# Performance work log

Hardware: AMD Instinct MI355X
Metric: run time of the kernel (lower is better)

## Reference

```python
import jax, jax.numpy as jnp
import numpy as np

B, S, H, NH, DW, V, W, L, NL = 8, 512, 768, 12, 300, 100000, 256, 4, 2


def _make_word_index(seed=0):
    # contiguous, non-overlapping spans of length 1..L starting at pos 1,
    # zero-padded at the end (matches the `break` on (0,0) in the original).
    rng = np.random.default_rng(seed)
    wi = np.zeros((B, W, 2), np.int32)
    for b in range(B):
        pos, w = 1, 0
        while w < W and pos < S:
            n = int(rng.integers(1, L + 1))
            end = min(pos + n, S)
            wi[b, w] = (pos, end)
            pos, w = end, w + 1
    return jnp.asarray(wi)


def _lin(key, din, dout):
    kw, _ = jax.random.split(key)
    return jax.random.normal(kw, (din, dout), jnp.float32) * 0.02, jnp.zeros((dout,), jnp.float32)


def setup_inputs() -> dict:
    key = jax.random.key(0)
    ks = jax.random.split(key, 14)
    tbl = jax.random.normal(ks[2], (V + 1, DW), jnp.float32) * 0.1
    tbl = tbl.at[V].set(0.0)  # appended zero row for OOV/pad
    d = dict(
        sequence_output=jax.random.normal(ks[0], (B, S, H), jnp.float32),
        word_ids=jax.random.randint(ks[1], (B, W), 0, V),
        word_index=_make_word_index(),
        word_table=tbl,
        mix_lambda=jnp.asarray(0.5, jnp.float32),
        mu=jnp.asarray(0.5, jnp.float32),
    )
    d['dt_w'], d['dt_b'] = _lin(ks[3], DW, H)
    d['dr_w'], d['dr_b'] = _lin(ks[4], H, H)
    d['q_w'], d['q_b'] = _lin(ks[5], H, H)
    d['k_w'], d['k_b'] = _lin(ks[6], H, H)
    d['v_w'], d['v_b'] = _lin(ks[7], H, H)
    d['qi_w'], d['qi_b'] = _lin(ks[8], H, H)
    d['ki_w'], d['ki_b'] = _lin(ks[9], H, H)
    d['vi_w'], d['vi_b'] = _lin(ks[10], H, H)
    d['fus_w'], d['fus_b'] = _lin(ks[11], H, H)
    d['dense_w'], d['dense_b'] = _lin(ks[12], H, H)
    d['cls_w'], d['cls_b'] = _lin(ks[13], H, NL)
    return d


def _mhsa(x, wq, bq, wk, bk, wv, bv, bias=None):
    b, s, h = x.shape
    hd = h // NH
    q = (x @ wq + bq).reshape(b, s, NH, hd).transpose(0, 2, 1, 3)
    k = (x @ wk + bk).reshape(b, s, NH, hd).transpose(0, 2, 1, 3)
    v = (x @ wv + bv).reshape(b, s, NH, hd).transpose(0, 2, 1, 3)
    scores = jnp.einsum('bhqd,bhkd->bhqk', q, k) / jnp.sqrt(jnp.asarray(hd, x.dtype))
    if bias is not None:
        scores = scores + bias
    p = jax.nn.softmax(scores, axis=-1)
    return jnp.einsum('bhqk,bhkd->bhqd', p, v).transpose(0, 2, 1, 3).reshape(b, s, h)


def _forward(sequence_output, word_ids, word_index, word_table, dt_w, dt_b, dr_w, dr_b,
             mix_lambda, mu, q_w, q_b, k_w, k_b, v_w, v_b, qi_w, qi_b, ki_w, ki_b,
             vi_w, vi_b, fus_w, fus_b, dense_w, dense_b, cls_w, cls_b):
    x = sequence_output
    # word embedding -> dim_transform -> tanh -> dim_retain
    we = jnp.tanh(word_table[word_ids] @ dt_w + dt_b) @ dr_w + dr_b  # [B,W,H]
    starts, ends = word_index[..., 0], word_index[..., 1]
    n = ends - starts                     # word lengths, 0 for padding
    valid_w = n > 0
    lpos = jnp.arange(L)
    pos = jnp.clip(starts[..., None] + lpos, 0, S - 1)              # [B,W,L]
    cvalid = (lpos[None, None, :] < n[..., None]) & valid_w[..., None]
    bidx = jnp.arange(B)[:, None, None]
    # char-word cosine similarity (computed on the ORIGINAL sequence_output)
    xg = x[bidx, pos]                                               # [B,W,L,H]
    xn = xg / jnp.linalg.norm(xg, axis=-1, keepdims=True)
    wen = we / jnp.linalg.norm(we, axis=-1, keepdims=True)
    cos = jnp.sum(xn * wen[:, :, None, :], axis=-1)                 # [B,W,L]
    cos_m = jnp.where(cvalid, cos, -1e9)
    # add softmax(cos)-weighted word embedding onto chars (scatter-add)
    sm = jax.nn.softmax(cos_m, axis=-1) * cvalid
    x1 = x.at[bidx, pos].add(sm[..., None] * we[:, :, None, :])
    # ragged mix: most-important char (mic) per word
    mic = jnp.argmax(cos_m, axis=-1)                                # [B,W]
    x1g = x1[bidx, pos]                                             # [B,W,L,H]
    x_mic = x1g[jnp.arange(B)[:, None], jnp.arange(W)[None, :], mic]  # [B,W,H]
    sum_x = jnp.sum(x1g * cvalid[..., None], axis=2)                # [B,W,H]
    f = jnp.exp(mix_lambda - 1.0)
    a = (1.0 - f) / jnp.maximum(n - 1, 1).astype(x.dtype)           # [B,W]
    mix_other = (1.0 - a[..., None, None]) * x1g + a[..., None, None] * x_mic[:, :, None, :]
    mix_mic = f * x_mic + a[..., None] * (sum_x - x_mic)
    is_mic = lpos[None, None, :] == mic[:, :, None]
    newv = jnp.where(is_mic[..., None], mix_mic[:, :, None, :], mix_other)
    mixmask = (cvalid & (n > 1)[..., None])[..., None].astype(x.dtype)
    x_mix = x1.at[bidx, pos].add((newv - x1g) * mixmask)
    # importance attention mask: only mic (or the single char) columns visible
    keep_pos = jnp.where(n == 1, starts, jnp.clip(starts + mic, 0, S - 1))
    keep = jnp.zeros((B, S), bool).at[jnp.arange(B)[:, None], keep_pos].max(valid_w)
    bias = jnp.where(keep[:, None, None, :], 0.0, -jnp.inf).astype(x.dtype)  # [B,1,1,S]
    h1 = _mhsa(x_mix, q_w, q_b, k_w, k_b, v_w, v_b, None)
    h2 = _mhsa(x_mix, qi_w, qi_b, ki_w, ki_b, vi_w, vi_b, bias)
    fus = jnp.tanh((mu * h1 + (1.0 - mu) * h2) @ fus_w + fus_b)
    pooled = jnp.tanh(fus[:, 0] @ dense_w + dense_b)                # CLS pooling
    return pooled @ cls_w + cls_b                                   # [B,NL]


def reference(sequence_output, word_ids, word_index, word_table, dt_w, dt_b, dr_w, dr_b,
              mix_lambda, mu, q_w, q_b, k_w, k_b, v_w, v_b, qi_w, qi_b, ki_w, ki_b,
              vi_w, vi_b, fus_w, fus_b, dense_w, dense_b, cls_w, cls_b):
    return _forward(sequence_output, word_ids, word_index, word_table, dt_w, dt_b, dr_w, dr_b,
                    mix_lambda, mu, q_w, q_b, k_w, k_b, v_w, v_b, qi_w, qi_b, ki_w, ki_b,
                    vi_w, vi_b, fus_w, fus_b, dense_w, dense_b, cls_w, cls_b)
```

## Files before the change

### kernel.cpp

```cpp
#include <hip/hip_runtime.h>
#include <math.h>

#define NB 8
#define SS 512
#define HH 768
#define NHD 12
#define HDIM 64
#define DWD 300
#define WW 256
#define LL 4
#define KC 6

__device__ __forceinline__ float waveReduceSum(float v){
    #pragma unroll
    for(int o=32;o>0;o>>=1) v += __shfl_xor(v,o,64);
    return v;
}

__global__ __launch_bounds__(256) void k_embed1f(const float* __restrict__ table,
        const int* __restrict__ ids, const float* __restrict__ Wm,
        const float* __restrict__ bias, float* __restrict__ out,
        int* __restrict__ keep,
        const float* __restrict__ x, const float* __restrict__ qw,
        const float* __restrict__ qiw, float* __restrict__ qpart){
    int bid = blockIdx.x;
    int t = threadIdx.x;
    if(bid >= 400){
        int rb = bid - 400;
        int kc = rb % KC;
        int jt = (rb/KC) % 3;
        int b  = rb / (KC*3);
        int j = jt*256 + t;
        const float* x0 = x + (size_t)b*SS*HH;
        int i0 = kc*128;
        float a1=0.f, a2=0.f;
        for(int i=i0;i<i0+128;i++){
            float xv = x0[i];
            a1 += xv*qw[(size_t)i*HH+j];
            a2 += xv*qiw[(size_t)i*HH+j];
        }
        qpart[(((size_t)kc*NB + b)*2 + 0)*HH + j] = a1;
        qpart[(((size_t)kc*NB + b)*2 + 1)*HH + j] = a2;
        return;
    }
    if(bid >= 384){
        int i = (bid-384)*256 + t;
        if(i < NB*SS) keep[i] = 0;
        return;
    }
    const int K=300, NT=19;
    __shared__ float As[16][68];
    __shared__ float Bs[16][68];
    int bx = bid % 12;
    int by = bid / 12;
    int m0 = by*64, n0 = bx*64;
    int tm = t>>4, tn = t&15;
    int lm = t>>2, lk = (t&3)*4;
    int kk = t>>4, c4 = (t&15)*4;
    int row_id = ids[m0+lm];
    const float* arow = table + (size_t)row_id*DWD;
    float acc[4][4] = {};
    float4 av, bv;
    if(lk < K) av = *(const float4*)&arow[lk]; else av = make_float4(0,0,0,0);
    if(kk < K) bv = *(const float4*)&Wm[(size_t)kk*HH + n0 + c4]; else bv = make_float4(0,0,0,0);
    for(int kt=0;kt<NT;kt++){
        __syncthreads();
        As[lk+0][lm]=av.x; As[lk+1][lm]=av.y; As[lk+2][lm]=av.z; As[lk+3][lm]=av.w;
        *(float4*)&Bs[kk][c4] = bv;
        __syncthreads();
        if(kt+1 < NT){
            int k0 = (kt+1)*16;
            if(k0+lk < K) av = *(const float4*)&arow[k0+lk]; else av = make_float4(0,0,0,0);
            if(k0+kk < K) bv = *(const float4*)&Wm[(size_t)(k0+kk)*HH + n0 + c4]; else bv = make_float4(0,0,0,0);
        }
        #pragma unroll
        for(int k=0;k<16;k++){
            float4 a = *(const float4*)&As[k][tm*4];
            float4 b = *(const float4*)&Bs[k][tn*4];
            acc[0][0]+=a.x*b.x; acc[0][1]+=a.x*b.y; acc[0][2]+=a.x*b.z; acc[0][3]+=a.x*b.w;
            acc[1][0]+=a.y*b.x; acc[1][1]+=a.y*b.y; acc[1][2]+=a.y*b.z; acc[1][3]+=a.y*b.w;
            acc[2][0]+=a.z*b.x; acc[2][1]+=a.z*b.y; acc[2][2]+=a.z*b.z; acc[2][3]+=a.z*b.w;
            acc[3][0]+=a.w*b.x; acc[3][1]+=a.w*b.y; acc[3][2]+=a.w*b.z; acc[3][3]+=a.w*b.w;
        }
    }
    #pragma unroll
    for(int i=0;i<4;i++){
        int m = m0 + tm*4 + i;
        int n = n0 + tn*4;
        float4 o;
        o.x = tanhf(acc[i][0] + bias[n+0]);
        o.y = tanhf(acc[i][1] + bias[n+1]);
        o.z = tanhf(acc[i][2] + bias[n+2]);
        o.w = tanhf(acc[i][3] + bias[n+3]);
        *(float4*)&out[(size_t)m*HH + n] = o;
    }
}

__global__ __launch_bounds__(256) void k_embed2f(const float* __restrict__ A,
        const float* __restrict__ Wm, const float* __restrict__ bias,
        float* __restrict__ out,
        const float4* __restrict__ xin4, float4* __restrict__ xmix4,
        const float* __restrict__ qpart,
        const float* __restrict__ qb, const float* __restrict__ qib,
        const float* __restrict__ kb, const float* __restrict__ kib,
        float* __restrict__ q0g, float* __restrict__ cst){
    int bid = blockIdx.x;
    int t = threadIdx.x;
    if(bid >= 3456){
        int b = bid - 3456;
        __shared__ float q0s[HH], qi0s[HH];
        for(int j=t;j<HH;j+=256){
            float a1=qb[j], a2=qib[j];
            #pragma unroll
            for(int kc=0;kc<KC;kc++){
                a1 += qpart[(((size_t)kc*NB+b)*2+0)*HH+j];
                a2 += qpart[(((size_t)kc*NB+b)*2+1)*HH+j];
            }
            q0s[j]=a1; qi0s[j]=a2;
            q0g[((size_t)b*2+0)*HH+j]=a1;
            q0g[((size_t)b*2+1)*HH+j]=a2;
        }
        __syncthreads();
        if(t<24){
            int slot=t, h=slot%NHD;
            const float* Kb = (slot<NHD)? kb:kib;
            const float* Q  = (slot<NHD)? q0s:qi0s;
            float a=0.f;
            for(int j=0;j<HDIM;j++) a += Kb[h*HDIM+j]*Q[h*HDIM+j];
            cst[b*24+slot]=a;
        }
        return;
    }
    if(bid >= 384){
        int i = (bid-384)*256 + t;
        xmix4[i] = xin4[i];
        return;
    }
    const int NT = 48;
    __shared__ float As[16][68];
    __shared__ float Bs[16][68];
    int bx = bid % 12;
    int by = bid / 12;
    int m0 = by*64, n0 = bx*64;
    int tm = t>>4, tn = t&15;
    int lm = t>>2, lk = (t&3)*4;
    int kk = t>>4, c4 = (t&15)*4;
    const float* arow = A + (size_t)(m0+lm)*HH;
    float acc[4][4] = {};
    float4 av = *(const float4*)&arow[lk];
    float4 bv = *(const float4*)&Wm[(size_t)kk*HH + n0 + c4];
    for(int kt=0;kt<NT;kt++){
        __syncthreads();
        As[lk+0][lm]=av.x; As[lk+1][lm]=av.y; As[lk+2][lm]=av.z; As[lk+3][lm]=av.w;
        *(float4*)&Bs[kk][c4] = bv;
        __syncthreads();
        if(kt+1 < NT){
            int k0 = (kt+1)*16;
            av = *(const float4*)&arow[k0+lk];
            bv = *(const float4*)&Wm[(size_t)(k0+kk)*HH + n0 + c4];
        }
        #pragma unroll
        for(int k=0;k<16;k++){
            float4 a = *(const float4*)&As[k][tm*4];
            float4 b = *(const float4*)&Bs[k][tn*4];
            acc[0][0]+=a.x*b.x; acc[0][1]+=a.x*b.y; acc[0][2]+=a.x*b.z; acc[0][3]+=a.x*b.w;
            acc[1][0]+=a.y*b.x; acc[1][1]+=a.y*b.y; acc[1][2]+=a.y*b.z; acc[1][3]+=a.y*b.w;
            acc[2][0]+=a.z*b.x; acc[2][1]+=a.z*b.y; acc[2][2]+=a.z*b.z; acc[2][3]+=a.z*b.w;
            acc[3][0]+=a.w*b.x; acc[3][1]+=a.w*b.y; acc[3][2]+=a.w*b.z; acc[3][3]+=a.w*b.w;
        }
    }
    #pragma unroll
    for(int i=0;i<4;i++){
        int m = m0 + tm*4 + i;
        int n = n0 + tn*4;
        float4 o;
        o.x = acc[i][0] + bias[n+0];
        o.y = acc[i][1] + bias[n+1];
        o.z = acc[i][2] + bias[n+2];
        o.w = acc[i][3] + bias[n+3];
        *(float4*)&out[(size_t)m*HH + n] = o;
    }
}

__global__ __launch_bounds__(256) void k_cosmix(const float* __restrict__ x,
        const int* __restrict__ wi, const float* __restrict__ we,
        const float* __restrict__ lam, int* __restrict__ keep,
        float* __restrict__ xmix,
        const float* __restrict__ q0g, const float* __restrict__ kw,
        const float* __restrict__ kiw, float* __restrict__ r){
    int bid = blockIdx.x;
    int t = threadIdx.x;
    if(bid >= 2048){
        int rb = bid - 2048;
        int ct = rb % 3;
        int slot = (rb/3) % 24;
        int b = rb / 72;
        int h = slot % NHD;
        __shared__ float qs[HDIM];
        const float* Q = q0g + ((size_t)b*2 + (slot<NHD?0:1))*HH + h*HDIM;
        if(t<HDIM) qs[t] = Q[t];
        __syncthreads();
        const float* K = (slot<NHD)? kw : kiw;
        int c = ct*256 + t;
        const float4* K4 = (const float4*)(K + (size_t)c*HH + h*HDIM);
        const float4* q4 = (const float4*)qs;
        float a=0.f;
        #pragma unroll
        for(int j=0;j<16;j++){
            float4 kv=K4[j], qv=q4[j];
            a += kv.x*qv.x + kv.y*qv.y + kv.z*qv.z + kv.w*qv.w;
        }
        r[((size_t)(b*24+slot))*HH + c] = a;
        return;
    }
    int bw = bid;
    int b = bw >> 8;
    int start = wi[bw*2+0];
    int end   = wi[bw*2+1];
    int n = end - start;
    if(n <= 0) return;
    __shared__ float weS[HH];
    __shared__ float xrow[LL][HH];
    __shared__ float cos_s[LL];
    int wv = t>>6, lane = t&63;
    const float* wer = we + (size_t)bw*HH;
    float wev[12];
    float wn = 0.f;
    #pragma unroll
    for(int i=0;i<12;i++){
        float v = wer[lane+64*i];
        wev[i]=v; wn += v*v;
        if(wv==0) weS[lane+64*i] = v;
    }
    wn = waveReduceSum(wn);
    if(wv < n){
        const float* xr = x + ((size_t)(b*SS + start + wv))*HH;
        float d=0.f, xs=0.f;
        #pragma unroll
        for(int i=0;i<12;i++){
            float xv = xr[lane+64*i];
            xrow[wv][lane+64*i] = xv;
            d += xv*wev[i]; xs += xv*xv;
        }
        d = waveReduceSum(d); xs = waveReduceSum(xs);
        if(lane==0) cos_s[wv] = d / sqrtf(xs*wn);
    } else {
        if(lane==0) cos_s[wv] = -1e9f;
    }
    __syncthreads();
    float c0=cos_s[0], c1=cos_s[1], c2=cos_s[2], c3=cos_s[3];
    float m = fmaxf(fmaxf(c0,c1),fmaxf(c2,c3));
    float e0 = (0<n)? expf(c0-m):0.f;
    float e1 = (1<n)? expf(c1-m):0.f;
    float e2 = (2<n)? expf(c2-m):0.f;
    float e3 = (3<n)? expf(c3-m):0.f;
    float inv = 1.f/(e0+e1+e2+e3);
    float s0=e0*inv, s1=e1*inv, s2=e2*inv, s3=e3*inv;
    int mic = 0; float bv = c0;
    if(c1 > bv){bv=c1;mic=1;}
    if(c2 > bv){bv=c2;mic=2;}
    if(c3 > bv){bv=c3;mic=3;}
    if(t==0) keep[b*SS + start + mic] = 1;
    float f = expf(lam[0] - 1.f);
    float a = (n>1)? (1.f-f)/(float)(n-1) : (1.f-f);
    for(int j=t; j<HH; j+=256){
        float wej = weS[j];
        float v0=0.f,v1=0.f,v2=0.f,v3=0.f;
        if(0<n) v0 = xrow[0][j] + s0*wej;
        if(1<n) v1 = xrow[1][j] + s1*wej;
        if(2<n) v2 = xrow[2][j] + s2*wej;
        if(3<n) v3 = xrow[3][j] + s3*wej;
        float sumx = v0+v1+v2+v3;
        float xm = (mic==0)?v0:(mic==1)?v1:(mic==2)?v2:v3;
        float mm = f*xm + a*(sumx-xm);
        if(0<n) xmix[((size_t)(b*SS+start+0))*HH+j] = (0==mic)? (n==1? v0 : mm) : ((1.f-a)*v0 + a*xm);
        if(1<n) xmix[((size_t)(b*SS+start+1))*HH+j] = (1==mic)? mm : ((1.f-a)*v1 + a*xm);
        if(2<n) xmix[((size_t)(b*SS+start+2))*HH+j] = (2==mic)? mm : ((1.f-a)*v2 + a*xm);
        if(3<n) xmix[((size_t)(b*SS+start+3))*HH+j] = (3==mic)? mm : ((1.f-a)*v3 + a*xm);
    }
}

__global__ __launch_bounds__(256) void k_scores(const float* __restrict__ xmix,
        const float* __restrict__ r, const float* __restrict__ cst,
        const int* __restrict__ keep, float* __restrict__ scores){
    int bs = blockIdx.x;
    int b = bs >> 9, s = bs & 511;
    __shared__ float xr[HH];
    for(int i=threadIdx.x;i<HH;i+=256) xr[i] = xmix[(size_t)bs*HH + i];
    __syncthreads();
    int wv = threadIdx.x>>6, lane = threadIdx.x&63;
    int kp = keep[b*SS + s];
    #pragma unroll
    for(int q=0;q<6;q++){
        int slot = wv*6 + q;
        const float* rr = r + ((size_t)(b*24+slot))*HH;
        float d = 0.f;
        #pragma unroll
        for(int i=0;i<12;i++) d += xr[lane+64*i]*rr[lane+64*i];
        d = waveReduceSum(d);
        if(lane==0){
            float sc = (d + cst[b*24+slot])*0.125f;
            if(slot>=12 && !kp) sc = -1e30f;
            scores[((size_t)(b*24+slot))*SS + s] = sc;
        }
    }
}

__global__ __launch_bounds__(256) void k_attn(const float* __restrict__ scores,
        const float* __restrict__ xmix, float* __restrict__ cg){
    int rb = blockIdx.x;
    int jt = rb % 3;
    int bslot = rb / 3;
    int b = bslot / 24, slot = bslot % 24;
    int t = threadIdx.x;
    __shared__ float p[SS];
    __shared__ float red[256];
    const float* srow = scores + (size_t)bslot*SS;
    float v0 = srow[t], v1 = srow[t+256];
    red[t] = fmaxf(v0,v1); __syncthreads();
    for(int o=128;o>0;o>>=1){ if(t<o) red[t] = fmaxf(red[t],red[t+o]); __syncthreads(); }
    float m = red[0]; __syncthreads();
    float e0 = expf(v0-m), e1 = expf(v1-m);
    red[t] = e0+e1; __syncthreads();
    for(int o=128;o>0;o>>=1){ if(t<o) red[t] += red[t+o]; __syncthreads(); }
    float inv = 1.f/red[0];
    p[t] = e0*inv; p[t+256] = e1*inv;
    __syncthreads();
    int j = jt*256 + t;
    const float* xb = xmix + (size_t)b*SS*HH + j;
    float a0 = 0.f;
    for(int s=0;s<SS;s++) a0 += p[s]*xb[(size_t)s*HH];
    cg[((size_t)bslot)*HH + j] = a0;
    (void)slot;
}

__global__ __launch_bounds__(256) void k_finA(const float* __restrict__ cg,
        const float* __restrict__ vw, const float* __restrict__ viw,
        const float* __restrict__ mu_, float* __restrict__ part){
    int kc = blockIdx.x % KC;
    int jt = (blockIdx.x/KC) % 3;
    int b  = blockIdx.x / (KC*3);
    int j = jt*256 + threadIdx.x;
    int h = j >> 6;
    float mu = mu_[0];
    const float* c1 = cg + ((size_t)(b*24+h))*HH;
    const float* c2 = cg + ((size_t)(b*24+12+h))*HH;
    int i0 = kc*128;
    float a1=0.f, a2=0.f;
    for(int i=i0;i<i0+128;i++){
        a1 += c1[i]*vw[(size_t)i*HH+j];
        a2 += c2[i]*viw[(size_t)i*HH+j];
    }
    part[((size_t)kc*NB+b)*HH + j] = mu*a1 + (1.f-mu)*a2;
}

__global__ __launch_bounds__(256) void k_finB(const float* __restrict__ part1,
        const float* __restrict__ vb, const float* __restrict__ vib,
        const float* __restrict__ mu_, const float* __restrict__ fw,
        float* __restrict__ part2){
    int kc = blockIdx.x % KC;
    int jt = (blockIdx.x/KC) % 3;
    int b  = blockIdx.x / (KC*3);
    int i0 = kc*128;
    int t = threadIdx.x;
    __shared__ float gs[128];
    if(t < 128){
        int i = i0 + t;
        float mu = mu_[0];
        float s = mu*vb[i] + (1.f-mu)*vib[i];
        #pragma unroll
        for(int k2=0;k2<KC;k2++) s += part1[((size_t)k2*NB+b)*HH + i];
        gs[t] = s;
    }
    __syncthreads();
    int j = jt*256 + t;
    float a = 0.f;
    for(int k=0;k<128;k++) a += gs[k]*fw[(size_t)(i0+k)*HH + j];
    part2[((size_t)kc*NB+b)*HH + j] = a;
}

__global__ __launch_bounds__(256) void k_finC(const float* __restrict__ part2,
        const float* __restrict__ fb, const float* __restrict__ dw,
        float* __restrict__ part1){
    int kc = blockIdx.x % KC;
    int jt = (blockIdx.x/KC) % 3;
    int b  = blockIdx.x / (KC*3);
    int i0 = kc*128;
    int t = threadIdx.x;
    __shared__ float fs[128];
    if(t < 128){
        int i = i0 + t;
        float s = fb[i];
        #pragma unroll
        for(int k2=0;k2<KC;k2++) s += part2[((size_t)k2*NB+b)*HH + i];
        fs[t] = tanhf(s);
    }
    __syncthreads();
    int j = jt*256 + t;
    float a = 0.f;
    for(int k=0;k<128;k++) a += fs[k]*dw[(size_t)(i0+k)*HH + j];
    part1[((size_t)kc*NB+b)*HH + j] = a;
}

__global__ __launch_bounds__(256) void k_finD(const float* __restrict__ part,
        const float* __restrict__ db, const float* __restrict__ cw,
        const float* __restrict__ cb, float* __restrict__ out){
    int b = blockIdx.x;
    int t = threadIdx.x;
    __shared__ float pooled[HH];
    __shared__ float red[256];
    for(int j=t;j<HH;j+=256){
        float s = db[j];
        #pragma unroll
        for(int kc=0;kc<KC;kc++) s += part[((size_t)kc*NB+b)*HH+j];
        pooled[j] = tanhf(s);
    }
    __syncthreads();
    float p0=0.f, p1=0.f;
    for(int i=t;i<HH;i+=256){ p0 += pooled[i]*cw[i*2+0]; p1 += pooled[i]*cw[i*2+1]; }
    red[t]=p0; __syncthreads();
    for(int o=128;o>0;o>>=1){ if(t<o) red[t]+=red[t+o]; __syncthreads(); }
    if(t==0) out[b*2+0] = red[0]+cb[0];
    __syncthreads();
    red[t]=p1; __syncthreads();
    for(int o=128;o>0;o>>=1){ if(t<o) red[t]+=red[t+o]; __syncthreads(); }
    if(t==0) out[b*2+1] = red[0]+cb[1];
}

extern "C" void kernel_launch(void* const* d_in, const int* in_sizes, int n_in,
                              void* d_out, int out_size, void* d_ws, size_t ws_size,
                              hipStream_t stream) {
    const float* x          = (const float*)d_in[0];
    const int*   word_ids   = (const int*)  d_in[1];
    const int*   word_index = (const int*)  d_in[2];
    const float* table      = (const float*)d_in[3];
    const float* lam        = (const float*)d_in[4];
    const float* mu         = (const float*)d_in[5];
    const float* dt_w = (const float*)d_in[6];
    const float* dt_b = (const float*)d_in[7];
    const float* dr_w = (const float*)d_in[8];
    const float* dr_b = (const float*)d_in[9];
    const float* q_w  = (const float*)d_in[10];
    const float* q_b  = (const float*)d_in[11];
    const float* k_w  = (const float*)d_in[12];
    const float* k_b  = (const float*)d_in[13];
    const float* v_w  = (const float*)d_in[14];
    const float* v_b  = (const float*)d_in[15];
    const float* qi_w = (const float*)d_in[16];
    const float* qi_b = (const float*)d_in[17];
    const float* ki_w = (const float*)d_in[18];
    const float* ki_b = (const float*)d_in[19];
    const float* vi_w = (const float*)d_in[20];
    const float* vi_b = (const float*)d_in[21];
    const float* fus_w = (const float*)d_in[22];
    const float* fus_b = (const float*)d_in[23];
    const float* dense_w = (const float*)d_in[24];
    const float* dense_b = (const float*)d_in[25];
    const float* cls_w = (const float*)d_in[26];
    const float* cls_b = (const float*)d_in[27];
    float* out = (float*)d_out;

    char* w = (char*)d_ws;
    float* xmix   = (float*)(w + 0);
    float* tbuf   = (float*)(w + 12582912);
    float* we     = (float*)(w + 18874368);
    float* scores = (float*)(w + 25165824);
    float* r      = (float*)(w + 25559040);
    float* cst    = (float*)(w + 26148864);
    int*   keep   = (int*)  (w + 26149888);
    float* cg     = (float*)(w + 26166272);
    float* qpart  = (float*)(w + 26756096);
    float* q0g    = (float*)(w + 27051008);
    float* part1  = (float*)(w + 27100160);
    float* part2  = (float*)(w + 27247616);
    (void)ws_size; (void)in_sizes; (void)n_in; (void)out_size;

    k_embed1f<<<544, 256, 0, stream>>>(table, word_ids, dt_w, dt_b, tbuf, keep,
                                       x, q_w, qi_w, qpart);
    k_embed2f<<<3464, 256, 0, stream>>>(tbuf, dr_w, dr_b, we,
                                        (const float4*)x, (float4*)xmix,
                                        qpart, q_b, qi_b, k_b, ki_b, q0g, cst);
    k_cosmix<<<2624, 256, 0, stream>>>(x, word_index, we, lam, keep, xmix,
                                       q0g, k_w, ki_w, r);
    k_scores<<<NB*SS, 256, 0, stream>>>(xmix, r, cst, keep, scores);
    k_attn<<<NB*24*3, 256, 0, stream>>>(scores, xmix, cg);
    k_finA<<<NB*3*KC, 256, 0, stream>>>(cg, v_w, vi_w, mu, part1);
    k_finB<<<NB*3*KC, 256, 0, stream>>>(part1, v_b, vi_b, mu, fus_w, part2);
    k_finC<<<NB*3*KC, 256, 0, stream>>>(part2, fus_b, dense_w, part1);
    k_finD<<<NB, 256, 0, stream>>>(part1, dense_b, cls_w, cls_b, out);
}
```

Before: 446.7 us.

## Share xmix reads across all 24 attention slots with sequence-split partials

```diff
diff --git a/kernel.cpp b/kernel.cpp
--- a/kernel.cpp
+++ b/kernel.cpp
@@ -10,10 +10,16 @@
 #define WW 256
 #define LL 4
 #define KC 6
+#define SC 8
 
 __device__ __forceinline__ float waveReduceSum(float v){
     #pragma unroll
     for(int o=32;o>0;o>>=1) v += __shfl_xor(v,o,64);
+    return v;
+}
+__device__ __forceinline__ float waveReduceMax(float v){
+    #pragma unroll
+    for(int o=32;o>0;o>>=1) v = fmaxf(v, __shfl_xor(v,o,64));
     return v;
 }
 
@@ -306,50 +312,79 @@
     }
 }
 
-__global__ __launch_bounds__(256) void k_attn(const float* __restrict__ scores,
-        const float* __restrict__ xmix, float* __restrict__ cg){
-    int rb = blockIdx.x;
-    int jt = rb % 3;
-    int bslot = rb / 3;
-    int b = bslot / 24, slot = bslot % 24;
-    int t = threadIdx.x;
-    __shared__ float p[SS];
-    __shared__ float red[256];
-    const float* srow = scores + (size_t)bslot*SS;
-    float v0 = srow[t], v1 = srow[t+256];
-    red[t] = fmaxf(v0,v1); __syncthreads();
-    for(int o=128;o>0;o>>=1){ if(t<o) red[t] = fmaxf(red[t],red[t+o]); __syncthreads(); }
-    float m = red[0]; __syncthreads();
-    float e0 = expf(v0-m), e1 = expf(v1-m);
-    red[t] = e0+e1; __syncthreads();
-    for(int o=128;o>0;o>>=1){ if(t<o) red[t] += red[t+o]; __syncthreads(); }
-    float inv = 1.f/red[0];
-    p[t] = e0*inv; p[t+256] = e1*inv;
+__global__ __launch_bounds__(256) void k_smc(const float* __restrict__ scores,
+        const float* __restrict__ xmix, float* __restrict__ cgp){
+    int bid = blockIdx.x;
+    int sc = bid & 7;
+    int jt = (bid>>3) % 3;
+    int b  = bid / 24;
+    int t = threadIdx.x;
+    int wv = t>>6, lane = t&63;
+    __shared__ float mstat[24], istat[24];
+    __shared__ float pchunk[24][64];
+    #pragma unroll
+    for(int q=0;q<6;q++){
+        int slot = wv*6 + q;
+        const float* srow = scores + ((size_t)(b*24+slot))*SS;
+        float mv = -3.4e38f;
+        #pragma unroll
+        for(int i=0;i<8;i++) mv = fmaxf(mv, srow[lane+64*i]);
+        mv = waveReduceMax(mv);
+        float sv = 0.f;
+        #pragma unroll
+        for(int i=0;i<8;i++) sv += expf(srow[lane+64*i] - mv);
+        sv = waveReduceSum(sv);
+        if(lane==0){ mstat[slot] = mv; istat[slot] = 1.f/sv; }
+    }
+    __syncthreads();
+    int s0 = sc*64;
+    for(int idx=t; idx<24*64; idx+=256){
+        int slot = idx>>6, ss = idx&63;
+        pchunk[slot][ss] = expf(scores[((size_t)(b*24+slot))*SS + s0+ss] - mstat[slot]) * istat[slot];
+    }
     __syncthreads();
     int j = jt*256 + t;
     const float* xb = xmix + (size_t)b*SS*HH + j;
-    float a0 = 0.f;
-    for(int s=0;s<SS;s++) a0 += p[s]*xb[(size_t)s*HH];
-    cg[((size_t)bslot)*HH + j] = a0;
-    (void)slot;
-}
-
-__global__ __launch_bounds__(256) void k_finA(const float* __restrict__ cg,
+    float acc[24];
+    #pragma unroll
+    for(int sl=0;sl<24;sl++) acc[sl] = 0.f;
+    for(int ss=0;ss<64;ss++){
+        float xv = xb[(size_t)(s0+ss)*HH];
+        #pragma unroll
+        for(int sl=0;sl<24;sl++) acc[sl] += pchunk[sl][ss]*xv;
+    }
+    #pragma unroll
+    for(int sl=0;sl<24;sl++)
+        cgp[(((size_t)sc*NB + b)*24 + sl)*HH + j] = acc[sl];
+}
+
+__global__ __launch_bounds__(256) void k_finA(const float* __restrict__ cgp,
         const float* __restrict__ vw, const float* __restrict__ viw,
         const float* __restrict__ mu_, float* __restrict__ part){
     int kc = blockIdx.x % KC;
     int jt = (blockIdx.x/KC) % 3;
     int b  = blockIdx.x / (KC*3);
-    int j = jt*256 + threadIdx.x;
-    int h = j >> 6;
+    int t = threadIdx.x;
+    int i0 = kc*128;
+    __shared__ float red[8][128];
+    for(int idx=t; idx<8*128; idx+=256){
+        int row = idx>>7, ii = idx&127;
+        int slot = (row<4)? (jt*4+row) : (jt*4+row-4+12);
+        float s = 0.f;
+        #pragma unroll
+        for(int sc2=0;sc2<SC;sc2++)
+            s += cgp[(((size_t)sc2*NB + b)*24 + slot)*HH + i0 + ii];
+        red[row][ii] = s;
+    }
+    __syncthreads();
+    int j = jt*256 + t;
+    int hh = (j>>6) - jt*4;
     float mu = mu_[0];
-    const float* c1 = cg + ((size_t)(b*24+h))*HH;
-    const float* c2 = cg + ((size_t)(b*24+12+h))*HH;
-    int i0 = kc*128;
     float a1=0.f, a2=0.f;
-    for(int i=i0;i<i0+128;i++){
-        a1 += c1[i]*vw[(size_t)i*HH+j];
-        a2 += c2[i]*viw[(size_t)i*HH+j];
+    for(int k=0;k<128;k++){
+        int i = i0 + k;
+        a1 += red[hh][k]  * vw[(size_t)i*HH+j];
+        a2 += red[hh+4][k]* viw[(size_t)i*HH+j];
     }
     part[((size_t)kc*NB+b)*HH + j] = mu*a1 + (1.f-mu)*a2;
 }
@@ -468,11 +503,11 @@
     float* r      = (float*)(w + 25559040);
     float* cst    = (float*)(w + 26148864);
     int*   keep   = (int*)  (w + 26149888);
-    float* cg     = (float*)(w + 26166272);
     float* qpart  = (float*)(w + 26756096);
     float* q0g    = (float*)(w + 27051008);
     float* part1  = (float*)(w + 27100160);
     float* part2  = (float*)(w + 27247616);
+    float* cgp    = (float*)(w + 27395072);
     (void)ws_size; (void)in_sizes; (void)n_in; (void)out_size;
 
     k_embed1f<<<544, 256, 0, stream>>>(table, word_ids, dt_w, dt_b, tbuf, keep,
@@ -483,8 +518,8 @@
     k_cosmix<<<2624, 256, 0, stream>>>(x, word_index, we, lam, keep, xmix,
                                        q0g, k_w, ki_w, r);
     k_scores<<<NB*SS, 256, 0, stream>>>(xmix, r, cst, keep, scores);
-    k_attn<<<NB*24*3, 256, 0, stream>>>(scores, xmix, cg);
-    k_finA<<<NB*3*KC, 256, 0, stream>>>(cg, v_w, vi_w, mu, part1);
+    k_smc<<<NB*3*SC, 256, 0, stream>>>(scores, xmix, cgp);
+    k_finA<<<NB*3*KC, 256, 0, stream>>>(cgp, v_w, vi_w, mu, part1);
     k_finB<<<NB*3*KC, 256, 0, stream>>>(part1, v_b, vi_b, mu, fus_w, part2);
     k_finC<<<NB*3*KC, 256, 0, stream>>>(part2, fus_b, dense_w, part1);
     k_finD<<<NB, 256, 0, stream>>>(part1, dense_b, cls_w, cls_b, out);
```

Result: faster. 412.2 us (-7.7%).
